# Kernel optimization log

Measured on AMD Instinct MI355X. Metric: run time of the kernel, lower is better.

## Reference

```python
import jax, jax.numpy as jnp
import numpy as np

B, D, K, N = 32, 512, 64, 4096
EPS = 1e-12


def setup_inputs() -> dict:
    key = jax.random.key(0)
    k1, k2, k3, k4 = jax.random.split(key, 4)
    featureVolume = jax.random.normal(k1, (B, D, N), dtype=jnp.float32)
    conv_w = jax.random.normal(k2, (K, D), dtype=jnp.float32) * (1.0 / np.sqrt(D))
    conv_b = jax.random.normal(k3, (K,), dtype=jnp.float32) * 0.01
    centers = jax.random.normal(k4, (D, K), dtype=jnp.float32)
    return {"featureVolume": featureVolume, "conv_w": conv_w, "conv_b": conv_b, "centers": centers}


def reference(featureVolume, conv_w, conv_b, centers):
    # 1x1 conv over length dim -> scores [B, K, N]
    scores = jnp.einsum('kd,bdn->bkn', conv_w, featureVolume) + conv_b[None, :, None]
    soft = jax.nn.softmax(scores, axis=1)                       # softmax over clusters K
    # VLAD aggregation without the B*D*K*N intermediate:
    # sum_n soft[b,k,n] * (x[b,d,n] - c[d,k])
    agg = jnp.einsum('bdn,bkn->bdk', featureVolume, soft)       # [B, D, K]
    agg = agg - centers[None, :, :] * jnp.sum(soft, axis=-1)[:, None, :]
    # intra-normalize over D (torch F.normalize, dim=1)
    norm1 = jnp.linalg.norm(agg, axis=1, keepdims=True)
    agg = agg / jnp.maximum(norm1, EPS)
    # flatten + global L2 normalize
    desc = agg.reshape(agg.shape[0], -1)                        # [B, D*K]
    norm2 = jnp.linalg.norm(desc, axis=1, keepdims=True)
    return desc / jnp.maximum(norm2, EPS)
```

## Files before the change

kernel.cpp:

```cpp
#include <hip/hip_runtime.h>
#include <hip/hip_bf16.h>

#define B_ 32
#define D_ 512
#define K_ 64
#define N_ 4096

typedef __attribute__((ext_vector_type(8))) short short8;
typedef __attribute__((ext_vector_type(4))) short short4v;
typedef __attribute__((ext_vector_type(4))) float f32x4;

static __device__ __forceinline__ unsigned short f2bf(float f) {
    __hip_bfloat16 h = __float2bfloat16(f);
    return *reinterpret_cast<unsigned short*>(&h);
}
static __device__ __forceinline__ float bf2f(unsigned short u) {
    return __uint_as_float(((unsigned)u) << 16);
}

#define SMEM_BYTES 156672
#define WL_OFF 0
#define XL_OFF 65536
#define XT_OFF 131072
#define PT_OFF 147456
#define SXC_OFF 155648

__global__ __launch_bounds__(512, 2) void vlad_fused(const float* __restrict__ X,
                                                     const float* __restrict__ W,
                                                     const float* __restrict__ bias,
                                                     float* __restrict__ aggs,
                                                     float* __restrict__ ssp) {
    extern __shared__ char smem[];
    char* WLp = smem + WL_OFF;
    char* XLp = smem + XL_OFF;
    char* XTp = smem + XT_OFF;
    char* PTp = smem + PT_OFF;
    float2* sxc = (float2*)(smem + SXC_OFF);

    const int ns = blockIdx.x;
    const int b  = blockIdx.y;
    const int t  = threadIdx.x;
    const int w  = t >> 6;
    const int l  = t & 63;
    const int lg = l >> 4;
    const int lr = l & 15;
    const int strip = w & 3;
    const int khalf = w >> 2;

    const int dq2 = t >> 4;
    const int nq  = t & 15;
    const float* Xbase = X + (size_t)b * D_ * N_ + ns * 512 + nq * 4;

    float4 Sa[4], Sb[4];
#pragma unroll
    for (int s = 0; s < 4; ++s) {
        const float* Xs = Xbase + (size_t)(s * 64 + dq2 * 2) * N_;
        Sa[s] = *(const float4*)&Xs[0];
        Sb[s] = *(const float4*)&Xs[N_];
    }

#pragma unroll 4
    for (int j = 0; j < 16; ++j) {
        const int idx = t + j * 512;
        const int k = idx >> 7;
        const int cf = idx & 127;
        const float4 wv = *(const float4*)&W[k * D_ + cf * 4];
        const int C = cf >> 1;
        const int swz = (C & ~7) | ((C ^ k) & 7);
        short4v pk;
        pk[0] = (short)f2bf(wv.x); pk[1] = (short)f2bf(wv.y);
        pk[2] = (short)f2bf(wv.z); pk[3] = (short)f2bf(wv.w);
        *(short4v*)(WLp + k * 1024 + (swz << 4) + (cf & 1) * 8) = pk;
    }

    float bias_r[2][4];
#pragma unroll
    for (int ktl = 0; ktl < 2; ++ktl)
#pragma unroll
        for (int r = 0; r < 4; ++r)
            bias_r[ktl][r] = bias[khalf * 32 + ktl * 16 + lg * 4 + r];

    f32x4 aacc[4][4];
#pragma unroll
    for (int m = 0; m < 4; ++m)
#pragma unroll
        for (int kt = 0; kt < 4; ++kt) {
            aacc[m][kt][0] = 0.f; aacc[m][kt][1] = 0.f;
            aacc[m][kt][2] = 0.f; aacc[m][kt][3] = 0.f;
        }
    float ssr[2][4];
#pragma unroll
    for (int ktl = 0; ktl < 2; ++ktl)
#pragma unroll
        for (int r = 0; r < 4; ++r) ssr[ktl][r] = 0.f;

    auto stage_write = [&](int buf, int dglob0, const float4& r0, const float4& r1) {
        const float e0[4] = {r0.x, r0.y, r0.z, r0.w};
        const float e1[4] = {r1.x, r1.y, r1.z, r1.w};
        {
            short4v pk;
            pk[0] = (short)f2bf(e0[0]); pk[1] = (short)f2bf(e0[1]);
            pk[2] = (short)f2bf(e0[2]); pk[3] = (short)f2bf(e0[3]);
            const int d = dglob0;
            *(short4v*)(XLp + d * 128 + ((((nq >> 1) ^ d) & 7) << 4) + (nq & 1) * 8) = pk;
        }
        {
            short4v pk;
            pk[0] = (short)f2bf(e1[0]); pk[1] = (short)f2bf(e1[1]);
            pk[2] = (short)f2bf(e1[2]); pk[3] = (short)f2bf(e1[3]);
            const int d = dglob0 + 1;
            *(short4v*)(XLp + d * 128 + ((((nq >> 1) ^ d) & 7) << 4) + (nq & 1) * 8) = pk;
        }
        const int C = dq2 >> 2;
#pragma unroll
        for (int c = 0; c < 4; ++c) {
            const int n = nq * 4 + c;
            const int sw = (C ^ (n & 7) ^ ((n >> 3) & 7)) & 7;
            const unsigned v = (unsigned)f2bf(e0[c]) | ((unsigned)f2bf(e1[c]) << 16);
            *(unsigned*)(XTp + buf * 8192 + n * 128 + (sw << 4) + (dq2 & 3) * 4) = v;
        }
    };

    __syncthreads();

    for (int nt = 0; nt < 8; ++nt) {
        const int base = nt * 8;

        stage_write(0, 0 * 64 + dq2 * 2, Sa[0], Sb[0]);
        {
            const int s4 = base + 4;
            if (s4 < 64) {
                const int nt2 = s4 >> 3, d2 = s4 & 7;
                const float* Xs = Xbase + nt2 * 64 + (size_t)(d2 * 64 + dq2 * 2) * N_;
                Sa[0] = *(const float4*)&Xs[0];
                Sb[0] = *(const float4*)&Xs[N_];
            }
        }
        __syncthreads();

        f32x4 sacc[2];
#pragma unroll
        for (int ktl = 0; ktl < 2; ++ktl) {
            sacc[ktl][0] = 0.f; sacc[ktl][1] = 0.f; sacc[ktl][2] = 0.f; sacc[ktl][3] = 0.f;
        }

#pragma unroll
        for (int dsl = 0; dsl < 8; ++dsl) {
            const int cur = dsl & 1;
            if (dsl < 7) {
                const int slot = (dsl + 1) & 3;
                stage_write(cur ^ 1, (dsl + 1) * 64 + dq2 * 2, Sa[slot], Sb[slot]);
                const int s5 = base + dsl + 5;
                if (s5 < 64) {
                    const int nt2 = s5 >> 3, d2 = s5 & 7;
                    const float* Xs = Xbase + nt2 * 64 + (size_t)(d2 * 64 + dq2 * 2) * N_;
                    Sa[slot] = *(const float4*)&Xs[0];
                    Sb[slot] = *(const float4*)&Xs[N_];
                }
            }
            const int n = strip * 16 + lr;
#pragma unroll
            for (int kc = 0; kc < 2; ++kc) {
                const int bC = kc * 4 + lg;
                const int sw = (bC ^ (n & 7) ^ ((n >> 3) & 7)) & 7;
                const short8 bfrag = *(const short8*)(XTp + cur * 8192 + n * 128 + (sw << 4));
#pragma unroll
                for (int ktl = 0; ktl < 2; ++ktl) {
                    const int k = khalf * 32 + ktl * 16 + lr;
                    const int aC = dsl * 8 + kc * 4 + lg;
                    const int swz = (aC & ~7) | ((aC ^ k) & 7);
                    const short8 afrag = *(const short8*)(WLp + k * 1024 + (swz << 4));
                    sacc[ktl] = __builtin_amdgcn_mfma_f32_16x16x32_bf16(afrag, bfrag, sacc[ktl], 0, 0, 0);
                }
            }
            if (dsl < 7) __syncthreads();
        }

        float p[2][4];
        float cw = -1e30f;
#pragma unroll
        for (int ktl = 0; ktl < 2; ++ktl)
#pragma unroll
            for (int r = 0; r < 4; ++r) {
                p[ktl][r] = sacc[ktl][r] + bias_r[ktl][r];
                cw = fmaxf(cw, p[ktl][r]);
            }
        cw = fmaxf(cw, __shfl_xor(cw, 16));
        cw = fmaxf(cw, __shfl_xor(cw, 32));
        float sum = 0.f;
#pragma unroll
        for (int ktl = 0; ktl < 2; ++ktl)
#pragma unroll
            for (int r = 0; r < 4; ++r) { p[ktl][r] = __expf(p[ktl][r] - cw); sum += p[ktl][r]; }
        sum += __shfl_xor(sum, 16);
        sum += __shfl_xor(sum, 32);
        if (l < 16) sxc[w * 16 + lr] = make_float2(cw, sum);
        __syncthreads();
        const float2 other = sxc[(w ^ 4) * 16 + lr];
        const float cstar = fmaxf(cw, other.x);
        const float e_own = __expf(cw - cstar);
        const float e_oth = __expf(other.x - cstar);
        const float scale = e_own / (sum * e_own + other.y * e_oth);

        {
            const int n = strip * 16 + lr;
#pragma unroll
            for (int ktl = 0; ktl < 2; ++ktl)
#pragma unroll
                for (int r = 0; r < 4; ++r) {
                    const int k = khalf * 32 + ktl * 16 + lg * 4 + r;
                    const unsigned short us = f2bf(p[ktl][r] * scale);
                    *(unsigned short*)(PTp + k * 128 + ((((n >> 3) ^ k) & 7) << 4) + (n & 7) * 2) = us;
                    ssr[ktl][r] += bf2f(us);
                }
        }
        __syncthreads();

#pragma unroll
        for (int kc = 0; kc < 2; ++kc) {
            const int aC = kc * 4 + lg;
            short8 bfr[4];
#pragma unroll
            for (int kt = 0; kt < 4; ++kt) {
                const int kk2 = kt * 16 + lr;
                bfr[kt] = *(const short8*)(PTp + kk2 * 128 + (((aC ^ kk2) & 7) << 4));
            }
#pragma unroll
            for (int m = 0; m < 4; ++m) {
                const int d = w * 64 + m * 16 + lr;
                const short8 afrag = *(const short8*)(XLp + d * 128 + (((aC ^ d) & 7) << 4));
#pragma unroll
                for (int kt = 0; kt < 4; ++kt)
                    aacc[m][kt] = __builtin_amdgcn_mfma_f32_16x16x32_bf16(afrag, bfr[kt], aacc[m][kt], 0, 0, 0);
            }
        }
        __syncthreads();
    }

    float* ag = aggs + ((size_t)ns * B_ + b) * (D_ * K_);
#pragma unroll
    for (int m = 0; m < 4; ++m)
#pragma unroll
        for (int kt = 0; kt < 4; ++kt)
#pragma unroll
            for (int r = 0; r < 4; ++r)
                ag[(size_t)(w * 64 + m * 16 + lg * 4 + r) * K_ + kt * 16 + lr] = aacc[m][kt][r];

#pragma unroll
    for (int ktl = 0; ktl < 2; ++ktl)
#pragma unroll
        for (int r = 0; r < 4; ++r) {
            float v = ssr[ktl][r];
            v += __shfl_xor(v, 1);
            v += __shfl_xor(v, 2);
            v += __shfl_xor(v, 4);
            v += __shfl_xor(v, 8);
            ssr[ktl][r] = v;
        }
    if (lr == 0) {
#pragma unroll
        for (int ktl = 0; ktl < 2; ++ktl)
#pragma unroll
            for (int r = 0; r < 4; ++r) {
                const int k = khalf * 32 + ktl * 16 + lg * 4 + r;
                ssp[(((size_t)b * 8 + ns) * 4 + strip) * K_ + k] = ssr[ktl][r];
            }
    }
}

__global__ __launch_bounds__(256) void vlad_norm1(const float* __restrict__ aggs,
                                                  const float* __restrict__ centers,
                                                  const float* __restrict__ ssp,
                                                  float* __restrict__ aggsum,
                                                  float* __restrict__ nrmp) {
    const int ds = blockIdx.x;
    const int b  = blockIdx.y;
    const int t  = threadIdx.x;
    const int k  = t & 63;
    const int dg = t >> 6;

    __shared__ float red[4][64];

    float s0 = 0.f;
#pragma unroll
    for (int j = 0; j < 8; ++j)
        s0 += ssp[((size_t)b * 32 + dg * 8 + j) * K_ + k];
    red[dg][k] = s0;
    __syncthreads();
    const float s = red[0][k] + red[1][k] + red[2][k] + red[3][k];
    __syncthreads();

    float sq = 0.f;
    for (int d = ds * 64 + dg; d < ds * 64 + 64; d += 4) {
        float v = -centers[d * K_ + k] * s;
#pragma unroll
        for (int i = 0; i < 8; ++i)
            v += aggs[((size_t)i * B_ + b) * (D_ * K_) + (size_t)d * K_ + k];
        aggsum[((size_t)b * D_ + d) * K_ + k] = v;
        sq = fmaf(v, v, sq);
    }
    red[dg][k] = sq;
    __syncthreads();
    if (t < 64) nrmp[((size_t)b * 8 + ds) * K_ + k] =
        red[0][k] + red[1][k] + red[2][k] + red[3][k];
}

__global__ __launch_bounds__(256) void vlad_norm2(const float* __restrict__ aggsum,
                                                  const float* __restrict__ nrmp,
                                                  float* __restrict__ out) {
    const int ds = blockIdx.x;
    const int b  = blockIdx.y;
    const int t  = threadIdx.x;
    const int k  = t & 63;
    const int dg = t >> 6;

    __shared__ float inv1s[64];
    __shared__ float col2[64];
    __shared__ float inv2s;

    if (t < 64) {
        float tt = 0.f;
#pragma unroll
        for (int i = 0; i < 8; ++i) tt += nrmp[((size_t)b * 8 + i) * K_ + k];
        const float n1 = sqrtf(tt);
        const float i1 = 1.f / fmaxf(n1, 1e-12f);
        inv1s[k] = i1;
        const float c2 = n1 * i1;
        col2[k] = c2 * c2;
    }
    __syncthreads();
    if (t == 0) {
        float tt = 0.f;
        for (int kk = 0; kk < 64; ++kk) tt += col2[kk];
        inv2s = 1.f / fmaxf(sqrtf(tt), 1e-12f);
    }
    __syncthreads();
    const float i12 = inv1s[k] * inv2s;
    for (int d = ds * 64 + dg; d < ds * 64 + 64; d += 4)
        out[(size_t)b * (D_ * K_) + (size_t)d * K_ + k] =
            aggsum[((size_t)b * D_ + d) * K_ + k] * i12;
}

extern "C" void kernel_launch(void* const* d_in, const int* in_sizes, int n_in,
                              void* d_out, int out_size, void* d_ws, size_t ws_size,
                              hipStream_t stream) {
    const float* X       = (const float*)d_in[0];
    const float* W       = (const float*)d_in[1];
    const float* bias    = (const float*)d_in[2];
    const float* centers = (const float*)d_in[3];
    float* out = (float*)d_out;

    char* ws = (char*)d_ws;
    const size_t aggBytes = (size_t)B_ * D_ * K_ * sizeof(float);
    float* aggs   = (float*)ws;
    float* aggsum = (float*)(ws + 8 * aggBytes);
    float* ssp    = (float*)(ws + 9 * aggBytes);
    float* nrmp   = (float*)(ws + 9 * aggBytes + 262144);

    hipFuncSetAttribute((const void*)vlad_fused,
                        hipFuncAttributeMaxDynamicSharedMemorySize, SMEM_BYTES);

    vlad_fused<<<dim3(8, B_), 512, SMEM_BYTES, stream>>>(X, W, bias, aggs, ssp);
    vlad_norm1<<<dim3(8, B_), 256, 0, stream>>>(aggs, centers, ssp, aggsum, nrmp);
    vlad_norm2<<<dim3(8, B_), 256, 0, stream>>>(aggsum, nrmp, out);
}
```

Before: 83.80 us.

## Fuse normalization kernels into main kernel using software grid barriers

```diff
diff --git a/kernel.cpp b/kernel.cpp
--- a/kernel.cpp
+++ b/kernel.cpp
@@ -5,6 +5,7 @@
 #define D_ 512
 #define K_ 64
 #define N_ 4096
+#define NBLK 256
 
 typedef __attribute__((ext_vector_type(8))) short short8;
 typedef __attribute__((ext_vector_type(4))) short short4v;
@@ -25,11 +26,26 @@
 #define PT_OFF 147456
 #define SXC_OFF 155648
 
+static __device__ __forceinline__ void gridbar(unsigned* cnt) {
+    __syncthreads();
+    if (threadIdx.x == 0) {
+        __threadfence();
+        atomicAdd(cnt, 1u);
+        while (atomicAdd(cnt, 0u) < (unsigned)NBLK) {}
+        __threadfence();
+    }
+    __syncthreads();
+}
+
 __global__ __launch_bounds__(512, 2) void vlad_fused(const float* __restrict__ X,
                                                      const float* __restrict__ W,
                                                      const float* __restrict__ bias,
+                                                     const float* __restrict__ centers,
                                                      float* __restrict__ aggs,
-                                                     float* __restrict__ ssp) {
+                                                     float* __restrict__ ssp,
+                                                     float* __restrict__ nrmp,
+                                                     float* __restrict__ out,
+                                                     unsigned* __restrict__ cnt) {
     extern __shared__ char smem[];
     char* WLp = smem + WL_OFF;
     char* XLp = smem + XL_OFF;
@@ -95,29 +111,26 @@
         for (int r = 0; r < 4; ++r) ssr[ktl][r] = 0.f;
 
     auto stage_write = [&](int buf, int dglob0, const float4& r0, const float4& r1) {
-        const float e0[4] = {r0.x, r0.y, r0.z, r0.w};
-        const float e1[4] = {r1.x, r1.y, r1.z, r1.w};
+        const unsigned short a0 = f2bf(r0.x), a1 = f2bf(r0.y), a2 = f2bf(r0.z), a3 = f2bf(r0.w);
+        const unsigned short b0 = f2bf(r1.x), b1 = f2bf(r1.y), b2 = f2bf(r1.z), b3 = f2bf(r1.w);
         {
-            short4v pk;
-            pk[0] = (short)f2bf(e0[0]); pk[1] = (short)f2bf(e0[1]);
-            pk[2] = (short)f2bf(e0[2]); pk[3] = (short)f2bf(e0[3]);
             const int d = dglob0;
-            *(short4v*)(XLp + d * 128 + ((((nq >> 1) ^ d) & 7) << 4) + (nq & 1) * 8) = pk;
+            *(uint2*)(XLp + d * 128 + ((((nq >> 1) ^ d) & 7) << 4) + (nq & 1) * 8) =
+                make_uint2((unsigned)a0 | ((unsigned)a1 << 16), (unsigned)a2 | ((unsigned)a3 << 16));
         }
         {
-            short4v pk;
-            pk[0] = (short)f2bf(e1[0]); pk[1] = (short)f2bf(e1[1]);
-            pk[2] = (short)f2bf(e1[2]); pk[3] = (short)f2bf(e1[3]);
             const int d = dglob0 + 1;
-            *(short4v*)(XLp + d * 128 + ((((nq >> 1) ^ d) & 7) << 4) + (nq & 1) * 8) = pk;
+            *(uint2*)(XLp + d * 128 + ((((nq >> 1) ^ d) & 7) << 4) + (nq & 1) * 8) =
+                make_uint2((unsigned)b0 | ((unsigned)b1 << 16), (unsigned)b2 | ((unsigned)b3 << 16));
         }
         const int C = dq2 >> 2;
+        const unsigned xv[4] = {(unsigned)a0 | ((unsigned)b0 << 16), (unsigned)a1 | ((unsigned)b1 << 16),
+                                (unsigned)a2 | ((unsigned)b2 << 16), (unsigned)a3 | ((unsigned)b3 << 16)};
 #pragma unroll
         for (int c = 0; c < 4; ++c) {
             const int n = nq * 4 + c;
             const int sw = (C ^ (n & 7) ^ ((n >> 3) & 7)) & 7;
-            const unsigned v = (unsigned)f2bf(e0[c]) | ((unsigned)f2bf(e1[c]) << 16);
-            *(unsigned*)(XTp + buf * 8192 + n * 128 + (sw << 4) + (dq2 & 3) * 4) = v;
+            *(unsigned*)(XTp + buf * 8192 + n * 128 + (sw << 4) + (dq2 & 3) * 4) = xv[c];
         }
     };
 
@@ -159,6 +172,7 @@
                 }
             }
             const int n = strip * 16 + lr;
+            __builtin_amdgcn_s_setprio(1);
 #pragma unroll
             for (int kc = 0; kc < 2; ++kc) {
                 const int bC = kc * 4 + lg;
@@ -173,6 +187,7 @@
                     sacc[ktl] = __builtin_amdgcn_mfma_f32_16x16x32_bf16(afrag, bfrag, sacc[ktl], 0, 0, 0);
                 }
             }
+            __builtin_amdgcn_s_setprio(0);
             if (dsl < 7) __syncthreads();
         }
 
@@ -216,6 +231,7 @@
         }
         __syncthreads();
 
+        __builtin_amdgcn_s_setprio(1);
 #pragma unroll
         for (int kc = 0; kc < 2; ++kc) {
             const int aC = kc * 4 + lg;
@@ -234,6 +250,7 @@
                     aacc[m][kt] = __builtin_amdgcn_mfma_f32_16x16x32_bf16(afrag, bfr[kt], aacc[m][kt], 0, 0, 0);
             }
         }
+        __builtin_amdgcn_s_setprio(0);
         __syncthreads();
     }
 
@@ -266,57 +283,50 @@
                 ssp[(((size_t)b * 8 + ns) * 4 + strip) * K_ + k] = ssr[ktl][r];
             }
     }
-}
-
-__global__ __launch_bounds__(256) void vlad_norm1(const float* __restrict__ aggs,
-                                                  const float* __restrict__ centers,
-                                                  const float* __restrict__ ssp,
-                                                  float* __restrict__ aggsum,
-                                                  float* __restrict__ nrmp) {
-    const int ds = blockIdx.x;
-    const int b  = blockIdx.y;
-    const int t  = threadIdx.x;
+
+    gridbar(cnt + 0);
+
+    const int ds = ns;
     const int k  = t & 63;
     const int dg = t >> 6;
-
-    __shared__ float red[4][64];
+    float* red8  = (float*)smem;
+    float* inv1s = (float*)(smem + 2048);
+    float* col2  = (float*)(smem + 2304);
+    float* inv2p = (float*)(smem + 2560);
 
     float s0 = 0.f;
 #pragma unroll
-    for (int j = 0; j < 8; ++j)
-        s0 += ssp[((size_t)b * 32 + dg * 8 + j) * K_ + k];
-    red[dg][k] = s0;
-    __syncthreads();
-    const float s = red[0][k] + red[1][k] + red[2][k] + red[3][k];
-    __syncthreads();
-
+    for (int j = 0; j < 4; ++j)
+        s0 += ssp[((size_t)b * 32 + dg * 4 + j) * K_ + k];
+    red8[dg * 64 + k] = s0;
+    __syncthreads();
+    float s = 0.f;
+#pragma unroll
+    for (int j = 0; j < 8; ++j) s += red8[j * 64 + k];
+    __syncthreads();
+
+    float vreg[8];
     float sq = 0.f;
-    for (int d = ds * 64 + dg; d < ds * 64 + 64; d += 4) {
+#pragma unroll
+    for (int j = 0; j < 8; ++j) {
+        const int d = ds * 64 + dg + j * 8;
         float v = -centers[d * K_ + k] * s;
 #pragma unroll
         for (int i = 0; i < 8; ++i)
             v += aggs[((size_t)i * B_ + b) * (D_ * K_) + (size_t)d * K_ + k];
-        aggsum[((size_t)b * D_ + d) * K_ + k] = v;
+        vreg[j] = v;
         sq = fmaf(v, v, sq);
     }
-    red[dg][k] = sq;
-    __syncthreads();
-    if (t < 64) nrmp[((size_t)b * 8 + ds) * K_ + k] =
-        red[0][k] + red[1][k] + red[2][k] + red[3][k];
-}
-
-__global__ __launch_bounds__(256) void vlad_norm2(const float* __restrict__ aggsum,
-                                                  const float* __restrict__ nrmp,
-                                                  float* __restrict__ out) {
-    const int ds = blockIdx.x;
-    const int b  = blockIdx.y;
-    const int t  = threadIdx.x;
-    const int k  = t & 63;
-    const int dg = t >> 6;
-
-    __shared__ float inv1s[64];
-    __shared__ float col2[64];
-    __shared__ float inv2s;
+    red8[dg * 64 + k] = sq;
+    __syncthreads();
+    if (t < 64) {
+        float tt = 0.f;
+#pragma unroll
+        for (int j = 0; j < 8; ++j) tt += red8[j * 64 + k];
+        nrmp[((size_t)b * 8 + ds) * K_ + k] = tt;
+    }
+
+    gridbar(cnt + 16);
 
     if (t < 64) {
         float tt = 0.f;
@@ -332,13 +342,15 @@
     if (t == 0) {
         float tt = 0.f;
         for (int kk = 0; kk < 64; ++kk) tt += col2[kk];
-        inv2s = 1.f / fmaxf(sqrtf(tt), 1e-12f);
-    }
-    __syncthreads();
-    const float i12 = inv1s[k] * inv2s;
-    for (int d = ds * 64 + dg; d < ds * 64 + 64; d += 4)
-        out[(size_t)b * (D_ * K_) + (size_t)d * K_ + k] =
-            aggsum[((size_t)b * D_ + d) * K_ + k] * i12;
+        inv2p[0] = 1.f / fmaxf(sqrtf(tt), 1e-12f);
+    }
+    __syncthreads();
+    const float i12 = inv1s[k] * inv2p[0];
+#pragma unroll
+    for (int j = 0; j < 8; ++j) {
+        const int d = ds * 64 + dg + j * 8;
+        out[(size_t)b * (D_ * K_) + (size_t)d * K_ + k] = vreg[j] * i12;
+    }
 }
 
 extern "C" void kernel_launch(void* const* d_in, const int* in_sizes, int n_in,
@@ -352,15 +364,15 @@
 
     char* ws = (char*)d_ws;
     const size_t aggBytes = (size_t)B_ * D_ * K_ * sizeof(float);
-    float* aggs   = (float*)ws;
-    float* aggsum = (float*)(ws + 8 * aggBytes);
-    float* ssp    = (float*)(ws + 9 * aggBytes);
-    float* nrmp   = (float*)(ws + 9 * aggBytes + 262144);
-
+    float*    aggs = (float*)ws;
+    float*    ssp  = (float*)(ws + 8 * aggBytes);
+    float*    nrmp = (float*)(ws + 8 * aggBytes + 262144);
+    unsigned* cnt  = (unsigned*)(ws + 8 * aggBytes + 262144 + 65536);
+
+    hipMemsetAsync(cnt, 0, 128, stream);
     hipFuncSetAttribute((const void*)vlad_fused,
                         hipFuncAttributeMaxDynamicSharedMemorySize, SMEM_BYTES);
 
-    vlad_fused<<<dim3(8, B_), 512, SMEM_BYTES, stream>>>(X, W, bias, aggs, ssp);
-    vlad_norm1<<<dim3(8, B_), 256, 0, stream>>>(aggs, centers, ssp, aggsum, nrmp);
-    vlad_norm2<<<dim3(8, B_), 256, 0, stream>>>(aggsum, nrmp, out);
-}
+    vlad_fused<<<dim3(8, B_), 512, SMEM_BYTES, stream>>>(X, W, bias, centers,
+                                                         aggs, ssp, nrmp, out, cnt);
+}
```

Result: slower. 126.2 us (+50.6%).
